# Performance work log

Hardware: AMD Instinct MI355X
Metric: run time of the kernel (lower is better)

## Reference

```python
import jax, jax.numpy as jnp
import numpy as np

B, C, H, W = 32, 3, 224, 224
P = 16
D = 768
HEADS, DH = 12, 64
INNER = HEADS * DH          # 768
DEPTH = 12
NUM_CLASSES = 1000
NP_ = (H // P) * (W // P)   # 196 patches
N = NP_ + 1                 # with cls token
PATCH_DIM = C * P * P       # 768
EPS = 1e-5


def _ln(x, g, b):
    mu = jnp.mean(x, axis=-1, keepdims=True)
    var = jnp.var(x, axis=-1, keepdims=True)
    return (x - mu) * jax.lax.rsqrt(var + EPS) * g + b


def setup_inputs() -> dict:
    key = jax.random.key(0)
    ks = jax.random.split(key, 16)
    s = 0.02
    return {
        "img": jax.random.normal(ks[0], (B, C, H, W), jnp.float32),
        "sph_dist": jax.random.uniform(ks[1], (N, N), jnp.float32),
        "patch_ln_g": jnp.ones((PATCH_DIM,), jnp.float32),
        "patch_ln_b": jnp.zeros((PATCH_DIM,), jnp.float32),
        "W_patch": jax.random.normal(ks[2], (PATCH_DIM, D), jnp.float32) * s,
        "b_patch": jnp.zeros((D,), jnp.float32),
        "emb_ln_g": jnp.ones((D,), jnp.float32),
        "emb_ln_b": jnp.zeros((D,), jnp.float32),
        "pos_emb": jax.random.normal(ks[3], (1, N, D), jnp.float32),
        "cls_tok": jax.random.normal(ks[4], (1, 1, D), jnp.float32),
        "ln_g": jnp.ones((DEPTH, D), jnp.float32),
        "ln_b": jnp.zeros((DEPTH, D), jnp.float32),
        "W_qkv": jax.random.normal(ks[5], (DEPTH, D, 3 * INNER), jnp.float32) * s,
        "W_out": jax.random.normal(ks[6], (DEPTH, INNER, D), jnp.float32) * s,
        "b_out": jnp.zeros((DEPTH, D), jnp.float32),
        "final_ln_g": jnp.ones((D,), jnp.float32),
        "final_ln_b": jnp.zeros((D,), jnp.float32),
        "W_head": jax.random.normal(ks[7], (D, NUM_CLASSES), jnp.float32) * s,
        "b_head": jnp.zeros((NUM_CLASSES,), jnp.float32),
    }


def _patchify(img):
    b = img.shape[0]
    # 'b c (h p1) (w p2) -> b (h w) (p1 p2 c)'
    x = img.reshape(b, C, H // P, P, W // P, P)
    x = x.transpose(0, 2, 4, 3, 5, 1)  # b h w p1 p2 c
    return x.reshape(b, NP_, PATCH_DIM)


def _attn_layer(x, sph_dist, g, bln, Wqkv, Wout, bout):
    b, n, _ = x.shape
    xn = _ln(x, g, bln)
    qkv = xn @ Wqkv                                  # [b,n,3*inner]
    q, k, v = jnp.split(qkv, 3, axis=-1)
    def heads(t):
        return t.reshape(b, n, HEADS, DH).transpose(0, 2, 1, 3)  # b h n d
    q, k, v = heads(q), heads(k), heads(v)
    dots = jnp.einsum('bhid,bhjd->bhij', q, k) * (DH ** -0.5)
    dw = dots * (1.0 + sph_dist)                     # broadcast over b,h
    mu = jnp.mean(dw, axis=1, keepdims=True)
    sd = jnp.std(dw, axis=1, keepdims=True, ddof=1)  # torch.std is unbiased
    dw = (dw - mu) / sd
    attn = jax.nn.softmax(dw, axis=-1)
    o = jnp.einsum('bhij,bhjd->bhid', attn, v)
    o = o.transpose(0, 2, 1, 3).reshape(b, n, INNER)
    return o @ Wout + bout


def reference(img, sph_dist, patch_ln_g, patch_ln_b, W_patch, b_patch,
              emb_ln_g, emb_ln_b, pos_emb, cls_tok,
              ln_g, ln_b, W_qkv, W_out, b_out,
              final_ln_g, final_ln_b, W_head, b_head):
    b = img.shape[0]
    x = _patchify(img)
    x = _ln(x, patch_ln_g, patch_ln_b)
    x = x @ W_patch + b_patch
    x = _ln(x, emb_ln_g, emb_ln_b)                   # [b, 196, D]
    cls = jnp.broadcast_to(cls_tok, (b, 1, D))
    x = jnp.concatenate([cls, x], axis=1)            # [b, 197, D]
    x = x + pos_emb[:, :x.shape[1]]
    for i in range(DEPTH):
        x = _attn_layer(x, sph_dist, ln_g[i], ln_b[i], W_qkv[i], W_out[i], b_out[i]) + x
    x = _ln(x, final_ln_g, final_ln_b)
    x = x[:, 0]                                      # cls pooling
    return x @ W_head + b_head
```

## Files before the change

### kernel.cpp

```cpp
#include <hip/hip_runtime.h>
#include <math.h>

constexpr int Bc = 32, Cch = 3, Hh = 224, Ww = 224, Pp = 16;
constexpr int Dd = 768, NH = 12, DHd = 64, INNERc = 768;
constexpr int DEPTHc = 12, NCLS = 1000;
constexpr int NPc = 196, Nn = 197, PD = 768;
constexpr float EPSf = 1e-5f;

typedef _Float16 half_t;
typedef __attribute__((ext_vector_type(8))) _Float16 half8;
typedef __attribute__((ext_vector_type(4))) float f32x4;
typedef __attribute__((ext_vector_type(4))) unsigned int uint32x4;

__device__ __forceinline__ float wave_red_sum(float v) {
#pragma unroll
    for (int m = 32; m; m >>= 1) v += __shfl_xor(v, m);
    return v;
}

__device__ __forceinline__ void block_red2(float& s, float& s2, float* red) {
    s = wave_red_sum(s);
    s2 = wave_red_sum(s2);
    int wid = threadIdx.x >> 6, lane = threadIdx.x & 63;
    if (lane == 0) { red[wid] = s; red[4 + wid] = s2; }
    __syncthreads();
    s = red[0] + red[1] + red[2] + red[3];
    s2 = red[4] + red[5] + red[6] + red[7];
}

__global__ __launch_bounds__(256) void k_patch_ln(
        const float* __restrict__ img, const float* __restrict__ g,
        const float* __restrict__ bb, half_t* __restrict__ out) {
    int pid = blockIdx.x;
    int b = pid / NPc, n = pid % NPc;
    int ph = n / 14, pw = n % 14;
    int t = threadIdx.x;
    __shared__ float red[8];
    float v[3];
#pragma unroll
    for (int i = 0; i < 3; i++) {
        int d = t + i * 256;
        int c = d % 3, q = (d / 3) & 15, p = d / 48;
        v[i] = img[((long)(b * Cch + c) * Hh + ph * Pp + p) * Ww + pw * Pp + q];
    }
    float s = v[0] + v[1] + v[2];
    float s2 = v[0] * v[0] + v[1] * v[1] + v[2] * v[2];
    block_red2(s, s2, red);
    float mu = s * (1.f / PD);
    float var = s2 * (1.f / PD) - mu * mu;
    float r = rsqrtf(var + EPSf);
#pragma unroll
    for (int i = 0; i < 3; i++) {
        int d = t + i * 256;
        out[(long)pid * PD + d] = (half_t)((v[i] - mu) * r * g[d] + bb[d]);
    }
}

template <typename T>
__global__ __launch_bounds__(256) void k_ln(
        const float* __restrict__ in, const float* __restrict__ g,
        const float* __restrict__ bb, T* __restrict__ out,
        long in_stride, long out_stride) {
    long row = blockIdx.x;
    const float* ip = in + row * in_stride;
    T* op = out + row * out_stride;
    int t = threadIdx.x;
    __shared__ float red[8];
    float v[3];
#pragma unroll
    for (int i = 0; i < 3; i++) v[i] = ip[t + i * 256];
    float s = v[0] + v[1] + v[2];
    float s2 = v[0] * v[0] + v[1] * v[1] + v[2] * v[2];
    block_red2(s, s2, red);
    float mu = s * (1.f / Dd);
    float var = s2 * (1.f / Dd) - mu * mu;
    float r = rsqrtf(var + EPSf);
#pragma unroll
    for (int i = 0; i < 3; i++) {
        int d = t + i * 256;
        op[d] = (T)((v[i] - mu) * r * g[d] + bb[d]);
    }
}

__global__ __launch_bounds__(256) void k_embed(
        const float* __restrict__ tmp, const float* __restrict__ cls,
        const float* __restrict__ pos, const float* __restrict__ g,
        const float* __restrict__ bb, float* __restrict__ x) {
    int pid = blockIdx.x;
    int b = pid / Nn, n = pid % Nn;
    int t = threadIdx.x;
    float* xp = x + (long)pid * Dd;
    if (n == 0) {
#pragma unroll
        for (int i = 0; i < 3; i++) {
            int d = t + i * 256;
            xp[d] = cls[d] + pos[d];
        }
        return;
    }
    const float* ip = tmp + (long)(b * NPc + n - 1) * Dd;
    __shared__ float red[8];
    float v[3];
#pragma unroll
    for (int i = 0; i < 3; i++) v[i] = ip[t + i * 256];
    float s = v[0] + v[1] + v[2];
    float s2 = v[0] * v[0] + v[1] * v[1] + v[2] * v[2];
    block_red2(s, s2, red);
    float mu = s * (1.f / Dd);
    float var = s2 * (1.f / Dd) - mu * mu;
    float r = rsqrtf(var + EPSf);
#pragma unroll
    for (int i = 0; i < 3; i++) {
        int d = t + i * 256;
        xp[d] = (v[i] - mu) * r * g[d] + bb[d] + pos[(long)n * Dd + d];
    }
}

__global__ __launch_bounds__(256) void k_wprep(
        const float* __restrict__ W, half_t* __restrict__ Wt, int K, int N) {
    W += (long)blockIdx.z * K * N;
    Wt += (long)blockIdx.z * K * N;
    __shared__ float tile[32][33];
    int n = blockIdx.x * 32 + threadIdx.x;
    int k0 = blockIdx.y * 32;
#pragma unroll
    for (int i = 0; i < 4; i++)
        tile[threadIdx.y + i * 8][threadIdx.x] = W[(long)(k0 + threadIdx.y + i * 8) * N + n];
    __syncthreads();
    int kk = k0 + threadIdx.x;
#pragma unroll
    for (int i = 0; i < 4; i++)
        Wt[(long)(blockIdx.x * 32 + threadIdx.y + i * 8) * K + kk] =
            (half_t)tile[threadIdx.x][threadIdx.y + i * 8];
}

__global__ __launch_bounds__(256) void k_wprep_head(
        const float* __restrict__ W, half_t* __restrict__ Wt) {
    __shared__ float tile[32][33];
    int n = blockIdx.x * 32 + threadIdx.x;
    int k0 = blockIdx.y * 32;
#pragma unroll
    for (int i = 0; i < 4; i++)
        tile[threadIdx.y + i * 8][threadIdx.x] =
            (n < NCLS) ? W[(long)(k0 + threadIdx.y + i * 8) * NCLS + n] : 0.f;
    __syncthreads();
    int kk = k0 + threadIdx.x;
#pragma unroll
    for (int i = 0; i < 4; i++)
        Wt[(long)(blockIdx.x * 32 + threadIdx.y + i * 8) * Dd + kk] =
            (half_t)tile[threadIdx.x][threadIdx.y + i * 8];
}

__global__ __launch_bounds__(256) void k_head(
        const half_t* __restrict__ Ah, const half_t* __restrict__ Wh,
        const float* __restrict__ bias, float* __restrict__ out) {
    int idx = blockIdx.x * 256 + threadIdx.x;
    int row = idx >> 10, col = idx & 1023;
    if (col >= NCLS) return;
    const half_t* ap = Ah + (long)row * Dd;
    const half_t* wp = Wh + (long)col * Dd;
    float acc = 0.f;
#pragma unroll
    for (int k = 0; k < 96; k++) {
        half8 a = *(const half8*)&ap[k * 8];
        half8 w = *(const half8*)&wp[k * 8];
#pragma unroll
        for (int u = 0; u < 8; u++) acc += (float)a[u] * (float)w[u];
    }
    out[(long)row * NCLS + col] = acc + bias[col];
}

__device__ __forceinline__ half8 lds_frag(const uint32x4 (*L)[8], int row, int slot) {
    union { uint32x4 u; half8 h; } t;
    t.u = L[row][slot];
    return t.h;
}

__device__ __forceinline__ void gload16(const half_t* g, uint32x4* l) {
    __builtin_amdgcn_global_load_lds(
        (const __attribute__((address_space(1))) unsigned int*)g,
        (__attribute__((address_space(3))) unsigned int*)l,
        16, 0, 0);
}

template <int HASB, int HASR, typename CT, int OMODE>
__global__ __launch_bounds__(256, 2) void k_hgemm(
        const half_t* __restrict__ A, const half_t* __restrict__ Bt,
        const float* __restrict__ bias, const float* __restrict__ res,
        CT* __restrict__ C, CT* __restrict__ C1, half_t* __restrict__ Vt,
        int M, int N, int K) {
    __shared__ uint32x4 smem[2176];
    uint32x4 (*As)[8] = (uint32x4(*)[8])smem;
    uint32x4 (*Bs)[8] = (uint32x4(*)[8])(smem + 1024);
    const int tid = threadIdx.x;
    const int nwg = gridDim.x;
    const int q8 = nwg >> 3, r8 = nwg & 7;
    const int xc = blockIdx.x & 7, oo = blockIdx.x >> 3;
    const int tile = (xc < r8 ? xc * (q8 + 1) : r8 * (q8 + 1) + (xc - r8) * q8) + oo;
    const int gx = N >> 7;
    const int n0 = (tile % gx) * 128, m0 = (tile / gx) * 128;
    const int lane = tid & 63, w = tid >> 6;
    const int wrr = (w >> 1) * 64, wcc = (w & 1) * 64;
    const int lrow = lane & 15, lgrp = lane >> 4;

    int ldsOff[4];
    long gsA[4], gsB[4];
#pragma unroll
    for (int c = 0; c < 4; ++c) {
        int r = w * 32 + c * 8 + (lane >> 3);
        int chunk = (lane & 7) ^ (r & 7);
        ldsOff[c] = (w * 32 + c * 8) * 8;
        gsA[c] = (long)min(m0 + r, M - 1) * K + chunk * 8;
        gsB[c] = (long)(n0 + r) * K + chunk * 8;
    }

    f32x4 acc[4][4] = {};

#define STAGE(k0)                                         \
    {                                                     \
        _Pragma("unroll")                                 \
        for (int c = 0; c < 4; ++c) {                     \
            gload16(A + gsA[c] + (k0), smem + ldsOff[c]); \
            gload16(Bt + gsB[c] + (k0), smem + 1024 + ldsOff[c]); \
        }                                                 \
    }

    STAGE(0);
    __syncthreads();

    const int nst = K >> 6;
    for (int t = 0; t < nst; ++t) {
#pragma unroll
        for (int kh = 0; kh < 2; ++kh) {
            half8 af[4], bf[4];
#pragma unroll
            for (int i2 = 0; i2 < 4; ++i2) {
                int m = wrr + i2 * 16 + lrow;
                af[i2] = lds_frag(As, m, (kh * 4 + lgrp) ^ (m & 7));
                int n = wcc + i2 * 16 + lrow;
                bf[i2] = lds_frag(Bs, n, (kh * 4 + lgrp) ^ (n & 7));
            }
#pragma unroll
            for (int i2 = 0; i2 < 4; ++i2)
#pragma unroll
                for (int j2 = 0; j2 < 4; ++j2)
                    acc[i2][j2] = __builtin_amdgcn_mfma_f32_16x16x32_f16(af[i2], bf[j2], acc[i2][j2], 0, 0, 0);
        }
        if (t + 1 < nst) {
            __syncthreads();
            STAGE((t + 1) << 6);
            __syncthreads();
        }
    }
#undef STAGE

    if constexpr (sizeof(CT) == 2) {
        if constexpr (OMODE == 1) {
            if (n0 >= 1536) {
                __syncthreads();
                half_t* Cs = (half_t*)smem;
#pragma unroll
                for (int i2 = 0; i2 < 4; ++i2)
#pragma unroll
                    for (int j2 = 0; j2 < 4; ++j2) {
                        int colc = wcc + j2 * 16 + lrow;
#pragma unroll
                        for (int q = 0; q < 4; ++q) {
                            int r = wrr + i2 * 16 + lgrp * 4 + q;
                            Cs[colc * 136 + r] = (half_t)acc[i2][j2][q];
                        }
                    }
                __syncthreads();
                const int rr = tid & 127;
                const int cbase = (tid >> 7) * 64;
                int token = m0 + rr;
                bool ok = token < M;
                int b = 0, nn = 0;
                if (ok) { b = token / Nn; nn = token - b * Nn; }
#pragma unroll
                for (int cc = 0; cc < 64; ++cc) {
                    int c = cbase + cc;
                    int rem = n0 + c - 1536;
                    int h = rem >> 6, d = rem & 63;
                    if (ok)
                        Vt[((long)(b * NH + h) * 64 + d) * 224 + nn] = Cs[c * 136 + rr];
                }
                return;
            }
        }
        __syncthreads();
        half_t* Cs = (half_t*)smem;
#pragma unroll
        for (int i2 = 0; i2 < 4; ++i2)
#pragma unroll
            for (int j2 = 0; j2 < 4; ++j2) {
                int colc = wcc + j2 * 16 + lrow;
                float bv = HASB ? bias[n0 + colc] : 0.f;
#pragma unroll
                for (int q = 0; q < 4; ++q) {
                    int r = wrr + i2 * 16 + lgrp * 4 + q;
                    Cs[r * 136 + colc] = (half_t)(acc[i2][j2][q] + bv);
                }
            }
        __syncthreads();
#pragma unroll
        for (int it = 0; it < 8; ++it) {
            int idx = tid + it * 256;
            int row = idx >> 4, cu = idx & 15;
            int token = m0 + row;
            if (token < M) {
                uint32x4 val = *(const uint32x4*)(Cs + row * 136 + cu * 8);
                if constexpr (OMODE == 1) {
                    int gc = n0 + cu * 8;
                    int which = gc >= 768 ? 1 : 0;
                    int rem = gc - which * 768;
                    int h = rem >> 6, d = rem & 63;
                    int b = token / Nn, nn = token - b * Nn;
                    CT* dst = (which == 0 ? C : C1);
                    __builtin_nontemporal_store(val,
                        (uint32x4*)(dst + (((long)(b * NH + h) * Nn + nn) << 6) + d));
                } else {
                    __builtin_nontemporal_store(val,
                        (uint32x4*)(C + (long)token * N + n0 + cu * 8));
                }
            }
        }
    } else {
#pragma unroll
        for (int i2 = 0; i2 < 4; ++i2)
#pragma unroll
            for (int j2 = 0; j2 < 4; ++j2) {
                int colc = n0 + wcc + j2 * 16 + lrow;
                float bv = HASB ? bias[colc] : 0.f;
#pragma unroll
                for (int q = 0; q < 4; ++q) {
                    int r = m0 + wrr + i2 * 16 + lgrp * 4 + q;
                    if (r < M) {
                        float v = acc[i2][j2][q] + bv;
                        if (HASR) v += res[(long)r * N + colc];
                        __builtin_nontemporal_store(v, &C[(long)r * N + colc]);
                    }
                }
            }
    }
}

__global__ __launch_bounds__(256) void k_stats(
        const half_t* __restrict__ qh, const half_t* __restrict__ kh,
        f32x4* __restrict__ muT, f32x4* __restrict__ rsT) {
    __shared__ f32x4 redv[2][64], redq[2][64];
    const int blk = (blockIdx.x & 7) * 338 + (blockIdx.x >> 3);
    const int w = threadIdx.x >> 6, lane = threadIdx.x & 63;
    const int ti = w >> 1, hh2 = w & 1;
    const int task = blk * 2 + ti;
    const int b = task / 169, r = task % 169;
    const int it = r / 13, jt = r % 13;
    const int lrow = lane & 15, lg = lane >> 4;
    const int i0 = it * 16, j0 = jt * 16;
    const int arow = min(i0 + lrow, Nn - 1);
    const int jr = min(j0 + lrow, Nn - 1);
    const int hbase = b * NH + hh2 * 6;

    float sv[4] = {}, sq[4] = {};
#pragma unroll
    for (int h = 0; h < 6; h++) {
        const half_t* Qp = qh + ((long)(hbase + h) * Nn) * 64;
        const half_t* Kp = kh + ((long)(hbase + h) * Nn) * 64;
        half8 af0 = *(const half8*)&Qp[(long)arow * 64 + lg * 8];
        half8 af1 = *(const half8*)&Qp[(long)arow * 64 + 32 + lg * 8];
        half8 bf0 = *(const half8*)&Kp[(long)jr * 64 + lg * 8];
        half8 bf1 = *(const half8*)&Kp[(long)jr * 64 + 32 + lg * 8];
        f32x4 acc = {};
        acc = __builtin_amdgcn_mfma_f32_16x16x32_f16(af0, bf0, acc, 0, 0, 0);
        acc = __builtin_amdgcn_mfma_f32_16x16x32_f16(af1, bf1, acc, 0, 0, 0);
#pragma unroll
        for (int q = 0; q < 4; q++) { sv[q] += acc[q]; sq[q] += acc[q] * acc[q]; }
    }
    if (hh2 == 1) {
        f32x4 a, b2;
#pragma unroll
        for (int q = 0; q < 4; q++) { a[q] = sv[q]; b2[q] = sq[q]; }
        redv[ti][lane] = a;
        redq[ti][lane] = b2;
    }
    __syncthreads();
    if (hh2 == 0) {
        f32x4 a = redv[ti][lane], b2 = redq[ti][lane];
        f32x4 muv, rsv;
#pragma unroll
        for (int q = 0; q < 4; q++) {
            float svt = sv[q] + a[q];
            float sqt = sq[q] + b2[q];
            float mu = svt * (1.f / NH);
            float var = (sqt - svt * mu) * (1.f / (NH - 1));
            muv[q] = mu;
            rsv[q] = rsqrtf(var);
        }
        long idx = ((long)(b * 13 + it) * 13 + jt) * 64 + lane;
        muT[idx] = muv;
        rsT[idx] = rsv;
    }
}

__global__ __launch_bounds__(128) void k_attn2(
        const half_t* __restrict__ qh, const half_t* __restrict__ kh,
        const half_t* __restrict__ vt, const f32x4* __restrict__ muT,
        const f32x4* __restrict__ rsT, half_t* __restrict__ o) {
    __shared__ half_t PB[16][232];
    __shared__ float xmx[2][16], xsm[2][16];
    const int tile = (blockIdx.x & 7) * 624 + (blockIdx.x >> 3);
    const int bh = tile / 13, it = tile % 13;
    const int b = bh / NH, h = bh % NH;
    const int i0 = it * 16;
    const int tid = threadIdx.x;
    const int wv = tid >> 6, lane = tid & 63;
    const int lrow = lane & 15, lg = lane >> 4;
    const int arow = min(i0 + lrow, Nn - 1);
    const int jtbase = wv * 7;
    const int njt = 7 - wv;

    if (wv == 0) {
        for (int idx = lane; idx < 128; idx += 64) {
            int rr = idx >> 3, u = idx & 7;
            *(unsigned int*)&PB[rr][208 + u * 2] = 0u;
        }
    }

    const half_t* Qp = qh + ((long)bh * Nn) * 64;
    const half_t* Kp = kh + ((long)bh * Nn) * 64;
    half8 af0 = *(const half8*)&Qp[(long)arow * 64 + lg * 8];
    half8 af1 = *(const half8*)&Qp[(long)arow * 64 + 32 + lg * 8];
    const f32x4* muB = muT + ((long)(b * 13 + it) * 13) * 64 + lane;
    const f32x4* rsB = rsT + ((long)(b * 13 + it) * 13) * 64 + lane;

    float ez[7][4];
    float mx[4] = {-1e30f, -1e30f, -1e30f, -1e30f};
#pragma unroll
    for (int jj = 0; jj < 7; jj++) {
        if (jj < njt) {
            int jt = jtbase + jj;
            int jr = min(jt * 16 + lrow, Nn - 1);
            half8 bf0 = *(const half8*)&Kp[(long)jr * 64 + lg * 8];
            half8 bf1 = *(const half8*)&Kp[(long)jr * 64 + 32 + lg * 8];
            f32x4 acc = {};
            acc = __builtin_amdgcn_mfma_f32_16x16x32_f16(af0, bf0, acc, 0, 0, 0);
            acc = __builtin_amdgcn_mfma_f32_16x16x32_f16(af1, bf1, acc, 0, 0, 0);
            f32x4 mu4 = muB[jt * 64];
            f32x4 rs4 = rsB[jt * 64];
            bool joob = (jt * 16 + lrow) > Nn - 1;
#pragma unroll
            for (int q = 0; q < 4; q++) {
                float z = (acc[q] - mu4[q]) * rs4[q];
                if (joob) z = -1e30f;
                ez[jj][q] = z;
                mx[q] = fmaxf(mx[q], z);
            }
        }
    }
#pragma unroll
    for (int st = 1; st <= 8; st <<= 1)
#pragma unroll
        for (int q = 0; q < 4; q++) mx[q] = fmaxf(mx[q], __shfl_xor(mx[q], st));
    if (lrow == 0) {
#pragma unroll
        for (int q = 0; q < 4; q++) xmx[wv][lg * 4 + q] = mx[q];
    }
    __syncthreads();
    float cmx[4];
#pragma unroll
    for (int q = 0; q < 4; q++)
        cmx[q] = fmaxf(xmx[0][lg * 4 + q], xmx[1][lg * 4 + q]);
    float sm[4] = {0.f, 0.f, 0.f, 0.f};
#pragma unroll
    for (int jj = 0; jj < 7; jj++) {
        if (jj < njt) {
#pragma unroll
            for (int q = 0; q < 4; q++) {
                float e = __expf(ez[jj][q] - cmx[q]);
                ez[jj][q] = e;
                sm[q] += e;
            }
        }
    }
#pragma unroll
    for (int st = 1; st <= 8; st <<= 1)
#pragma unroll
        for (int q = 0; q < 4; q++) sm[q] += __shfl_xor(sm[q], st);
    if (lrow == 0) {
#pragma unroll
        for (int q = 0; q < 4; q++) xsm[wv][lg * 4 + q] = sm[q];
    }
    __syncthreads();
    float inv[4];
#pragma unroll
    for (int q = 0; q < 4; q++)
        inv[q] = 1.f / (xsm[0][lg * 4 + q] + xsm[1][lg * 4 + q]);
#pragma unroll
    for (int jj = 0; jj < 7; jj++) {
        if (jj < njt) {
#pragma unroll
            for (int q = 0; q < 4; q++)
                PB[lg * 4 + q][(jtbase + jj) * 16 + lrow] = (half_t)(ez[jj][q] * inv[q]);
        }
    }
    __syncthreads();

    const half_t* Vtp = vt + ((long)bh * 64) * 224;
#pragma unroll
    for (int dd = 0; dd < 2; dd++) {
        int dt = wv * 2 + dd;
        f32x4 oacc = {};
#pragma unroll
        for (int kt = 0; kt < 7; kt++) {
            half8 pa = *(const half8*)&PB[lrow][kt * 32 + lg * 8];
            half8 vb = *(const half8*)&Vtp[(long)(dt * 16 + lrow) * 224 + kt * 32 + lg * 8];
            oacc = __builtin_amdgcn_mfma_f32_16x16x32_f16(pa, vb, oacc, 0, 0, 0);
        }
#pragma unroll
        for (int q = 0; q < 4; q++) {
            int i = i0 + lg * 4 + q;
            if (i < Nn)
                o[((long)(b * Nn) + i) * INNERc + h * 64 + dt * 16 + lrow] = (half_t)oacc[q];
        }
    }
}

extern "C" void kernel_launch(void* const* d_in, const int* in_sizes, int n_in,
                              void* d_out, int out_size, void* d_ws, size_t ws_size,
                              hipStream_t stream) {
    const float* img     = (const float*)d_in[0];
    const float* patch_g = (const float*)d_in[2];
    const float* patch_b = (const float*)d_in[3];
    const float* W_patch = (const float*)d_in[4];
    const float* b_patch = (const float*)d_in[5];
    const float* emb_g   = (const float*)d_in[6];
    const float* emb_b   = (const float*)d_in[7];
    const float* pos     = (const float*)d_in[8];
    const float* cls     = (const float*)d_in[9];
    const float* ln_g    = (const float*)d_in[10];
    const float* ln_b    = (const float*)d_in[11];
    const float* W_qkv   = (const float*)d_in[12];
    const float* W_out   = (const float*)d_in[13];
    const float* b_out   = (const float*)d_in[14];
    const float* fin_g   = (const float*)d_in[15];
    const float* fin_b   = (const float*)d_in[16];
    const float* W_head  = (const float*)d_in[17];
    const float* b_head  = (const float*)d_in[18];
    float* out = (float*)d_out;

    const long SZ_XD  = (long)Bc * Nn * Dd;
    const long SZ_HD  = (long)Bc * NH * Nn * DHd;
    const long SZ_VT  = (long)Bc * NH * 64 * 224;
    const long SZ_TMP = (long)Bc * NPc * Dd;
    const long SZ_MU  = (long)Bc * 169 * 256 + 1024;

    float* x    = (float*)d_ws;
    float* tmp  = x + SZ_XD;
    float* muG  = tmp + SZ_TMP;
    float* rsG  = muG + SZ_MU;
    half_t* xh       = (half_t*)(rsG + SZ_MU);
    half_t* qhb      = xh + SZ_XD;
    half_t* khb      = qhb + SZ_HD;
    half_t* vtb      = khb + SZ_HD;
    half_t* clsh     = vtb + SZ_VT;
    half_t* wh_head  = clsh + 32 * Dd;
    half_t* wt_patch = wh_head + 1024 * Dd;
    half_t* wt_qkv   = wt_patch + (long)Dd * Dd;
    half_t* wt_out   = wt_qkv + (long)DEPTHc * 3 * INNERc * Dd;

    hipLaunchKernelGGL(k_wprep, dim3(Dd / 32, Dd / 32, 1), dim3(32, 8), 0, stream,
                       W_patch, wt_patch, Dd, Dd);
    hipLaunchKernelGGL(k_wprep, dim3(3 * INNERc / 32, Dd / 32, DEPTHc), dim3(32, 8), 0, stream,
                       W_qkv, wt_qkv, Dd, 3 * INNERc);
    hipLaunchKernelGGL(k_wprep, dim3(Dd / 32, Dd / 32, DEPTHc), dim3(32, 8), 0, stream,
                       W_out, wt_out, Dd, Dd);
    hipLaunchKernelGGL(k_wprep_head, dim3(32, 24), dim3(32, 8), 0, stream,
                       W_head, wh_head);

    hipLaunchKernelGGL(k_patch_ln, dim3(Bc * NPc), dim3(256), 0, stream,
                       img, patch_g, patch_b, xh);
    hipLaunchKernelGGL((k_hgemm<1, 0, float, 0>), dim3(6 * 49), dim3(256), 0, stream,
                       xh, wt_patch, b_patch, nullptr,
                       tmp, nullptr, nullptr, Bc * NPc, Dd, Dd);
    hipLaunchKernelGGL(k_embed, dim3(Bc * Nn), dim3(256), 0, stream,
                       tmp, cls, pos, emb_g, emb_b, x);

    const int Mrows = Bc * Nn;
    for (int l = 0; l < DEPTHc; l++) {
        const float* g  = ln_g + (long)l * Dd;
        const float* bb = ln_b + (long)l * Dd;
        const half_t* Wq = wt_qkv + (long)l * 3 * INNERc * Dd;
        const half_t* Wo = wt_out + (long)l * Dd * Dd;
        const float* bo = b_out + (long)l * Dd;
        hipLaunchKernelGGL((k_ln<half_t>), dim3(Mrows), dim3(256), 0, stream,
                           x, g, bb, xh, (long)Dd, (long)Dd);
        hipLaunchKernelGGL((k_hgemm<0, 0, half_t, 1>), dim3(18 * 50), dim3(256), 0, stream,
                           xh, Wq, nullptr, nullptr,
                           qhb, khb, vtb, Mrows, 3 * INNERc, Dd);
        hipLaunchKernelGGL(k_stats, dim3(2704), dim3(256), 0, stream,
                           qhb, khb, (f32x4*)muG, (f32x4*)rsG);
        hipLaunchKernelGGL(k_attn2, dim3(4992), dim3(128), 0, stream,
                           qhb, khb, vtb, (const f32x4*)muG, (const f32x4*)rsG, xh);
        hipLaunchKernelGGL((k_hgemm<1, 1, float, 0>), dim3(6 * 50), dim3(256), 0, stream,
                           xh, Wo, bo, x,
                           x, nullptr, nullptr, Mrows, Dd, Dd);
    }
    hipLaunchKernelGGL((k_ln<half_t>), dim3(Bc), dim3(256), 0, stream,
                       x, fin_g, fin_b, clsh, (long)Nn * Dd, (long)Dd);
    hipLaunchKernelGGL(k_head, dim3(128), dim3(256), 0, stream,
                       clsh, wh_head, b_head, out);
}
```

Measured before the change: 1.670 ms.

## Store normalized attention scores in stats kernel instead of recomputing QK^T

Result: faster. 1.585 ms (-5.1%).

```diff
diff --git a/kernel.cpp b/kernel.cpp
--- a/kernel.cpp
+++ b/kernel.cpp
@@ -347,8 +347,8 @@
 
 __global__ __launch_bounds__(256) void k_stats(
         const half_t* __restrict__ qh, const half_t* __restrict__ kh,
-        f32x4* __restrict__ muT, f32x4* __restrict__ rsT) {
-    __shared__ f32x4 redv[2][64], redq[2][64];
+        half_t* __restrict__ Z) {
+    __shared__ f32x4 redv[2][2][64], redq[2][2][64];
     const int blk = (blockIdx.x & 7) * 338 + (blockIdx.x >> 3);
     const int w = threadIdx.x >> 6, lane = threadIdx.x & 63;
     const int ti = w >> 1, hh2 = w & 1;
@@ -361,6 +361,7 @@
     const int jr = min(j0 + lrow, Nn - 1);
     const int hbase = b * NH + hh2 * 6;
 
+    float sAll[6][4];
     float sv[4] = {}, sq[4] = {};
 #pragma unroll
     for (int h = 0; h < 6; h++) {
@@ -374,38 +375,42 @@
         acc = __builtin_amdgcn_mfma_f32_16x16x32_f16(af0, bf0, acc, 0, 0, 0);
         acc = __builtin_amdgcn_mfma_f32_16x16x32_f16(af1, bf1, acc, 0, 0, 0);
 #pragma unroll
-        for (int q = 0; q < 4; q++) { sv[q] += acc[q]; sq[q] += acc[q] * acc[q]; }
-    }
-    if (hh2 == 1) {
-        f32x4 a, b2;
-#pragma unroll
-        for (int q = 0; q < 4; q++) { a[q] = sv[q]; b2[q] = sq[q]; }
-        redv[ti][lane] = a;
-        redq[ti][lane] = b2;
-    }
-    __syncthreads();
-    if (hh2 == 0) {
-        f32x4 a = redv[ti][lane], b2 = redq[ti][lane];
-        f32x4 muv, rsv;
-#pragma unroll
         for (int q = 0; q < 4; q++) {
-            float svt = sv[q] + a[q];
-            float sqt = sq[q] + b2[q];
-            float mu = svt * (1.f / NH);
-            float var = (sqt - svt * mu) * (1.f / (NH - 1));
-            muv[q] = mu;
-            rsv[q] = rsqrtf(var);
-        }
-        long idx = ((long)(b * 13 + it) * 13 + jt) * 64 + lane;
-        muT[idx] = muv;
-        rsT[idx] = rsv;
+            sAll[h][q] = acc[q];
+            sv[q] += acc[q];
+            sq[q] += acc[q] * acc[q];
+        }
+    }
+    f32x4 a, b2;
+#pragma unroll
+    for (int q = 0; q < 4; q++) { a[q] = sv[q]; b2[q] = sq[q]; }
+    redv[ti][hh2][lane] = a;
+    redq[ti][hh2][lane] = b2;
+    __syncthreads();
+    f32x4 oa = redv[ti][hh2 ^ 1][lane], ob = redq[ti][hh2 ^ 1][lane];
+    float mu[4], rs[4];
+#pragma unroll
+    for (int q = 0; q < 4; q++) {
+        float svt = sv[q] + oa[q];
+        float sqt = sq[q] + ob[q];
+        mu[q] = svt * (1.f / NH);
+        float var = (sqt - svt * mu[q]) * (1.f / (NH - 1));
+        rs[q] = rsqrtf(var);
+    }
+    half_t* zp = Z + (((long)task * NH + hh2 * 6) * 64 + lane) * 4;
+#pragma unroll
+    for (int h = 0; h < 6; h++) {
+        union { unsigned long long u; half_t hv[4]; } t;
+#pragma unroll
+        for (int q = 0; q < 4; q++)
+            t.hv[q] = (half_t)((sAll[h][q] - mu[q]) * rs[q]);
+        *(unsigned long long*)(zp + (long)h * 256) = t.u;
     }
 }
 
 __global__ __launch_bounds__(128) void k_attn2(
-        const half_t* __restrict__ qh, const half_t* __restrict__ kh,
-        const half_t* __restrict__ vt, const f32x4* __restrict__ muT,
-        const f32x4* __restrict__ rsT, half_t* __restrict__ o) {
+        const half_t* __restrict__ Z, const half_t* __restrict__ vt,
+        half_t* __restrict__ o) {
     __shared__ half_t PB[16][232];
     __shared__ float xmx[2][16], xsm[2][16];
     const int tile = (blockIdx.x & 7) * 624 + (blockIdx.x >> 3);
@@ -415,7 +420,6 @@
     const int tid = threadIdx.x;
     const int wv = tid >> 6, lane = tid & 63;
     const int lrow = lane & 15, lg = lane >> 4;
-    const int arow = min(i0 + lrow, Nn - 1);
     const int jtbase = wv * 7;
     const int njt = 7 - wv;
 
@@ -426,31 +430,19 @@
         }
     }
 
-    const half_t* Qp = qh + ((long)bh * Nn) * 64;
-    const half_t* Kp = kh + ((long)bh * Nn) * 64;
-    half8 af0 = *(const half8*)&Qp[(long)arow * 64 + lg * 8];
-    half8 af1 = *(const half8*)&Qp[(long)arow * 64 + 32 + lg * 8];
-    const f32x4* muB = muT + ((long)(b * 13 + it) * 13) * 64 + lane;
-    const f32x4* rsB = rsT + ((long)(b * 13 + it) * 13) * 64 + lane;
-
+    const long taskbase = (long)b * 169 + it * 13;
     float ez[7][4];
     float mx[4] = {-1e30f, -1e30f, -1e30f, -1e30f};
 #pragma unroll
     for (int jj = 0; jj < 7; jj++) {
         if (jj < njt) {
             int jt = jtbase + jj;
-            int jr = min(jt * 16 + lrow, Nn - 1);
-            half8 bf0 = *(const half8*)&Kp[(long)jr * 64 + lg * 8];
-            half8 bf1 = *(const half8*)&Kp[(long)jr * 64 + 32 + lg * 8];
-            f32x4 acc = {};
-            acc = __builtin_amdgcn_mfma_f32_16x16x32_f16(af0, bf0, acc, 0, 0, 0);
-            acc = __builtin_amdgcn_mfma_f32_16x16x32_f16(af1, bf1, acc, 0, 0, 0);
-            f32x4 mu4 = muB[jt * 64];
-            f32x4 rs4 = rsB[jt * 64];
+            union { unsigned long long u; half_t hv[4]; } t;
+            t.u = *(const unsigned long long*)(Z + (((taskbase + jt) * NH + h) * 64 + lane) * 4);
             bool joob = (jt * 16 + lrow) > Nn - 1;
 #pragma unroll
             for (int q = 0; q < 4; q++) {
-                float z = (acc[q] - mu4[q]) * rs4[q];
+                float z = (float)t.hv[q];
                 if (joob) z = -1e30f;
                 ez[jj][q] = z;
                 mx[q] = fmaxf(mx[q], z);
@@ -552,17 +544,16 @@
     const long SZ_HD  = (long)Bc * NH * Nn * DHd;
     const long SZ_VT  = (long)Bc * NH * 64 * 224;
     const long SZ_TMP = (long)Bc * NPc * Dd;
-    const long SZ_MU  = (long)Bc * 169 * 256 + 1024;
+    const long SZ_Z   = (long)Bc * 169 * NH * 256;
 
     float* x    = (float*)d_ws;
     float* tmp  = x + SZ_XD;
-    float* muG  = tmp + SZ_TMP;
-    float* rsG  = muG + SZ_MU;
-    half_t* xh       = (half_t*)(rsG + SZ_MU);
+    half_t* xh       = (half_t*)(tmp + SZ_TMP);
     half_t* qhb      = xh + SZ_XD;
     half_t* khb      = qhb + SZ_HD;
     half_t* vtb      = khb + SZ_HD;
-    half_t* clsh     = vtb + SZ_VT;
+    half_t* Zb       = vtb + SZ_VT;
+    half_t* clsh     = Zb + SZ_Z;
     half_t* wh_head  = clsh + 32 * Dd;
     half_t* wt_patch = wh_head + 1024 * Dd;
     half_t* wt_qkv   = wt_patch + (long)Dd * Dd;
@@ -598,9 +589,9 @@
                            xh, Wq, nullptr, nullptr,
                            qhb, khb, vtb, Mrows, 3 * INNERc, Dd);
         hipLaunchKernelGGL(k_stats, dim3(2704), dim3(256), 0, stream,
-                           qhb, khb, (f32x4*)muG, (f32x4*)rsG);
+                           qhb, khb, Zb);
         hipLaunchKernelGGL(k_attn2, dim3(4992), dim3(128), 0, stream,
-                           qhb, khb, vtb, (const f32x4*)muG, (const f32x4*)rsG, xh);
+                           Zb, vtb, xh);
         hipLaunchKernelGGL((k_hgemm<1, 1, float, 0>), dim3(6 * 50), dim3(256), 0, stream,
                            xh, Wo, bo, x,
                            x, nullptr, nullptr, Mrows, Dd, Dd);
```
